# Optimization experiments

Hardware: AMD Instinct MI355X
Metric: run time of the kernel (lower is better)

The kernel has to match this reference:

```python
import jax, jax.numpy as jnp
import numpy as np

N, NPER, B, E = 65536, 1024, 64, 1048576
IN_F, HID, K, NCLS = 128, 64, 16, 10


def setup_inputs() -> dict:
    key = jax.random.key(0)
    ks = jax.random.split(key, 12)
    x = jax.random.normal(ks[0], (N, IN_F), jnp.float32)
    # block-structured intra-graph edges: 64 graphs of 1024 contiguous nodes
    gid = jax.random.randint(ks[1], (E,), 0, B)
    src = gid * NPER + jax.random.randint(ks[2], (E,), 0, NPER)
    dst = gid * NPER + jax.random.randint(ks[3], (E,), 0, NPER)
    edge_index = jnp.stack([src, dst]).astype(jnp.int32)
    batch = (jnp.arange(N, dtype=jnp.int32) // NPER).astype(jnp.int32)
    def lin(k, fo, fi):
        kw, kb = jax.random.split(k)
        s = 1.0 / np.sqrt(fi)
        return (jax.random.uniform(kw, (fo, fi), jnp.float32, -s, s),
                jax.random.uniform(kb, (fo,), jnp.float32, -s, s))
    W1, b1 = lin(ks[4], HID, IN_F)
    W2, b2 = lin(ks[5], HID, HID)
    Wp, bp = lin(ks[6], K, HID)      # DMoN cluster-assignment MLP (single Linear)
    Wl, bl = lin(ks[7], NCLS, HID)   # final classifier
    return {"x": x, "edge_index": edge_index, "batch": batch,
            "W1": W1, "b1": b1, "W2": W2, "b2": b2,
            "Wp": Wp, "bp": bp, "Wl": Wl, "bl": bl}


def gcn_conv(x, src, dst, W, b):
    # GCNConv with add_self_loops=True, symmetric normalization
    n = x.shape[0]
    deg = jax.ops.segment_sum(jnp.ones(src.shape[0], x.dtype), dst,
                              num_segments=n) + 1.0  # +1 for self-loop
    dinv = jax.lax.rsqrt(deg)
    h = x @ W.T
    coef = (dinv[src] * dinv[dst])[:, None]
    agg = jax.ops.segment_sum(h[src] * coef, dst, num_segments=n)
    agg = agg + h * (dinv * dinv)[:, None]  # self-loop contribution
    return agg + b


def reference(x, edge_index, batch, W1, b1, W2, b2, Wp, bp, Wl, bl):
    src, dst = edge_index[0], edge_index[1]
    h = jax.nn.relu(gcn_conv(x, src, dst, W1, b1))
    h = jax.nn.relu(gcn_conv(h, src, dst, W2, b2))
    # to_dense_batch: graphs are equal-sized and contiguous -> reshape, mask all True
    Xb = h.reshape(B, NPER, HID)
    # DMoN cluster assignment (dropout=0.0, mask all ones)
    s = jax.nn.softmax(Xb @ Wp.T + bp, axis=-1)          # [B, NPER, K]
    Xp = jax.nn.selu(jnp.einsum('bnk,bnh->bkh', s, Xb))   # pooled clusters [B, K, HID]
    out = Xp.mean(axis=1)                                  # [B, HID]
    logits = out @ Wl.T + bl                               # [B, NCLS]
    return logits
```

## Files before the change

### kernel.cpp

```cpp
#include <hip/hip_runtime.h>
#include <cstddef>

#define N_NODES 65536
#define NPER    1024
#define NGRAPH  64
#define HID     64
#define IN_F    128
#define KCLUS   16
#define NCLS    10
#define ECAP    18432
#define HSTRIDE 12

__global__ __launch_bounds__(256) void bucket_kernel(const int* __restrict__ src,
                                                     const int* __restrict__ dst,
                                                     int* __restrict__ ecnt,
                                                     int* __restrict__ gedges, int E) {
    __shared__ int hist[NGRAPH];
    __shared__ int base_l[NGRAPH];
    const int t = threadIdx.x;
    const int e0 = blockIdx.x * 1024;
    if (t < NGRAPH) hist[t] = 0;
    __syncthreads();

    int gg[4], rr[4], pk[4];
#pragma unroll
    for (int i = 0; i < 4; ++i) {
        int idx = e0 + i * 256 + t;
        if (idx < E) {
            int d = dst[idx], s = src[idx];
            int g = d >> 10;
            gg[i] = g;
            pk[i] = ((d & 1023) << 10) | (s & 1023);
            rr[i] = atomicAdd(&hist[g], 1);
        } else gg[i] = -1;
    }
    __syncthreads();
    if (t < NGRAPH) base_l[t] = atomicAdd(&ecnt[t], hist[t]);
    __syncthreads();
#pragma unroll
    for (int i = 0; i < 4; ++i) {
        if (gg[i] >= 0) {
            int pos = base_l[gg[i]] + rr[i];
            if (pos < ECAP) gedges[gg[i] * ECAP + pos] = pk[i];
        }
    }
}

__global__ __launch_bounds__(1024) void csr_kernel(const int* __restrict__ gedges,
                                                   const int* __restrict__ ecnt,
                                                   int* __restrict__ rp,
                                                   unsigned short* __restrict__ esorted,
                                                   float* __restrict__ dinv) {
    __shared__ int hist[NPER];
    __shared__ int wsum[16];
    const int g = blockIdx.x, t = threadIdx.x;
    const int lane = t & 63, wid = t >> 6;
    const int ec = ecnt[g];
    const int* ge = gedges + (size_t)g * ECAP;

    hist[t] = 0;
    __syncthreads();
    for (int i = t; i < ec; i += 1024) atomicAdd(&hist[ge[i] >> 10], 1);
    __syncthreads();

    const int h0 = hist[t];
    int v = h0;
#pragma unroll
    for (int off = 1; off < 64; off <<= 1) {
        int x = __shfl_up(v, off, 64);
        if (lane >= off) v += x;
    }
    if (lane == 63) wsum[wid] = v;
    __syncthreads();
    if (wid == 0) {
        int wv = (lane < 16) ? wsum[lane] : 0;
#pragma unroll
        for (int off = 1; off < 16; off <<= 1) {
            int x = __shfl_up(wv, off, 64);
            if (lane >= off) wv += x;
        }
        if (lane < 16) wsum[lane] = wv;
    }
    __syncthreads();
    const int incl = v + (wid > 0 ? wsum[wid - 1] : 0);
    const int excl = incl - h0;

    rp[g * (NPER + 1) + t] = excl;
    if (t == NPER - 1) rp[g * (NPER + 1) + NPER] = incl;
    dinv[g * NPER + t] = rsqrtf((float)h0 + 1.0f);

    hist[t] = excl;
    __syncthreads();

    unsigned short* es = esorted + (size_t)g * ECAP;
    for (int i = t; i < ec; i += 1024) {
        int pk = ge[i];
        int pos = atomicAdd(&hist[pk >> 10], 1);
        es[pos] = (unsigned short)(pk & 1023);
    }
}

template <int K>
__global__ __launch_bounds__(256) void linear_kernel(const float* __restrict__ X,
                                                     const float* __restrict__ W,
                                                     float* __restrict__ Y) {
    __shared__ float xsT[64][68];
    __shared__ float wsT[64][68];
    const int t = threadIdx.x;
    const size_t row0 = (size_t)blockIdx.x * 64;
    const int r0 = (t >> 4) * 4;
    const int c0 = (t & 15) * 4;
    float acc[4][4] = {};

    for (int kc = 0; kc < K; kc += 64) {
        __syncthreads();
        for (int i = t; i < 1024; i += 256) {
            int row = i >> 4, k4 = (i & 15) << 2;
            float4 v = *(const float4*)(X + (row0 + row) * K + kc + k4);
            xsT[k4 + 0][row] = v.x;
            xsT[k4 + 1][row] = v.y;
            xsT[k4 + 2][row] = v.z;
            xsT[k4 + 3][row] = v.w;
        }
        for (int i = t; i < 1024; i += 256) {
            int col = i >> 4, k4 = (i & 15) << 2;
            float4 v = *(const float4*)(W + col * K + kc + k4);
            wsT[k4 + 0][col] = v.x;
            wsT[k4 + 1][col] = v.y;
            wsT[k4 + 2][col] = v.z;
            wsT[k4 + 3][col] = v.w;
        }
        __syncthreads();

#pragma unroll 8
        for (int k = 0; k < 64; ++k) {
            float4 xv = *(const float4*)&xsT[k][r0];
            float4 wv = *(const float4*)&wsT[k][c0];
            acc[0][0] = fmaf(xv.x, wv.x, acc[0][0]);
            acc[0][1] = fmaf(xv.x, wv.y, acc[0][1]);
            acc[0][2] = fmaf(xv.x, wv.z, acc[0][2]);
            acc[0][3] = fmaf(xv.x, wv.w, acc[0][3]);
            acc[1][0] = fmaf(xv.y, wv.x, acc[1][0]);
            acc[1][1] = fmaf(xv.y, wv.y, acc[1][1]);
            acc[1][2] = fmaf(xv.y, wv.z, acc[1][2]);
            acc[1][3] = fmaf(xv.y, wv.w, acc[1][3]);
            acc[2][0] = fmaf(xv.z, wv.x, acc[2][0]);
            acc[2][1] = fmaf(xv.z, wv.y, acc[2][1]);
            acc[2][2] = fmaf(xv.z, wv.z, acc[2][2]);
            acc[2][3] = fmaf(xv.z, wv.w, acc[2][3]);
            acc[3][0] = fmaf(xv.w, wv.x, acc[3][0]);
            acc[3][1] = fmaf(xv.w, wv.y, acc[3][1]);
            acc[3][2] = fmaf(xv.w, wv.z, acc[3][2]);
            acc[3][3] = fmaf(xv.w, wv.w, acc[3][3]);
        }
    }

#pragma unroll
    for (int i = 0; i < 4; ++i) {
        float4 v = make_float4(acc[i][0], acc[i][1], acc[i][2], acc[i][3]);
        *(float4*)(Y + (row0 + r0 + i) * HID + c0) = v;
    }
}

__global__ __launch_bounds__(512) void agg_kernel(const float* __restrict__ h,
                                                  const unsigned short* __restrict__ esorted,
                                                  const int* __restrict__ rp,
                                                  const float* __restrict__ dinv,
                                                  const float* __restrict__ bias,
                                                  float* __restrict__ outp) {
    __shared__ float Hs[NPER * HSTRIDE];
    __shared__ float dl[NPER];
    const int g = blockIdx.x >> 3;
    const int f0 = (blockIdx.x & 7) * 8;
    const int t = threadIdx.x;
    const int base = g * NPER;

    for (int r = t; r < NPER; r += 512) {
        const float* hp = h + (size_t)(base + r) * HID + f0;
        float4 a = *(const float4*)hp;
        float4 b = *(const float4*)(hp + 4);
        float dv = dinv[base + r];
        dl[r] = dv;
        float* row = &Hs[r * HSTRIDE];
        *(float4*)row = make_float4(a.x * dv, a.y * dv, a.z * dv, a.w * dv);
        *(float4*)(row + 4) = make_float4(b.x * dv, b.y * dv, b.z * dv, b.w * dv);
    }
    float bb[8];
#pragma unroll
    for (int j = 0; j < 8; ++j) bb[j] = bias[f0 + j];
    const unsigned short* es = esorted + (size_t)g * ECAP;
    const int* rpg = rp + g * (NPER + 1);
    __syncthreads();

    for (int ld = t; ld < NPER; ld += 512) {
        int p = rpg[ld];
        const int pe = rpg[ld + 1];
        const float* srow = &Hs[ld * HSTRIDE];
        float4 acc0 = *(const float4*)srow;
        float4 acc1 = *(const float4*)(srow + 4);
        float4 bcc0 = make_float4(0.f, 0.f, 0.f, 0.f);
        float4 bcc1 = make_float4(0.f, 0.f, 0.f, 0.f);

        for (; p + 4 <= pe; p += 4) {
            const float* r0 = &Hs[(int)es[p + 0] * HSTRIDE];
            const float* r1 = &Hs[(int)es[p + 1] * HSTRIDE];
            const float* r2 = &Hs[(int)es[p + 2] * HSTRIDE];
            const float* r3 = &Hs[(int)es[p + 3] * HSTRIDE];
            float4 a0 = *(const float4*)r0, a1 = *(const float4*)(r0 + 4);
            float4 b0 = *(const float4*)r1, b1 = *(const float4*)(r1 + 4);
            float4 c0v = *(const float4*)r2, c1v = *(const float4*)(r2 + 4);
            float4 d0 = *(const float4*)r3, d1 = *(const float4*)(r3 + 4);
            acc0.x += a0.x; acc0.y += a0.y; acc0.z += a0.z; acc0.w += a0.w;
            acc1.x += a1.x; acc1.y += a1.y; acc1.z += a1.z; acc1.w += a1.w;
            bcc0.x += b0.x; bcc0.y += b0.y; bcc0.z += b0.z; bcc0.w += b0.w;
            bcc1.x += b1.x; bcc1.y += b1.y; bcc1.z += b1.z; bcc1.w += b1.w;
            acc0.x += c0v.x; acc0.y += c0v.y; acc0.z += c0v.z; acc0.w += c0v.w;
            acc1.x += c1v.x; acc1.y += c1v.y; acc1.z += c1v.z; acc1.w += c1v.w;
            bcc0.x += d0.x; bcc0.y += d0.y; bcc0.z += d0.z; bcc0.w += d0.w;
            bcc1.x += d1.x; bcc1.y += d1.y; bcc1.z += d1.z; bcc1.w += d1.w;
        }
        for (; p < pe; ++p) {
            const float* rw = &Hs[(int)es[p] * HSTRIDE];
            float4 a = *(const float4*)rw;
            float4 b = *(const float4*)(rw + 4);
            acc0.x += a.x; acc0.y += a.y; acc0.z += a.z; acc0.w += a.w;
            acc1.x += b.x; acc1.y += b.y; acc1.z += b.z; acc1.w += b.w;
        }
        acc0.x += bcc0.x; acc0.y += bcc0.y; acc0.z += bcc0.z; acc0.w += bcc0.w;
        acc1.x += bcc1.x; acc1.y += bcc1.y; acc1.z += bcc1.z; acc1.w += bcc1.w;

        const float dv = dl[ld];
        float4 o0, o1;
        o0.x = fmaxf(fmaf(acc0.x, dv, bb[0]), 0.f);
        o0.y = fmaxf(fmaf(acc0.y, dv, bb[1]), 0.f);
        o0.z = fmaxf(fmaf(acc0.z, dv, bb[2]), 0.f);
        o0.w = fmaxf(fmaf(acc0.w, dv, bb[3]), 0.f);
        o1.x = fmaxf(fmaf(acc1.x, dv, bb[4]), 0.f);
        o1.y = fmaxf(fmaf(acc1.y, dv, bb[5]), 0.f);
        o1.z = fmaxf(fmaf(acc1.z, dv, bb[6]), 0.f);
        o1.w = fmaxf(fmaf(acc1.w, dv, bb[7]), 0.f);
        float* op = outp + (size_t)(base + ld) * HID + f0;
        *(float4*)op = o0;
        *(float4*)(op + 4) = o1;
    }
}

__global__ __launch_bounds__(256) void pool1_kernel(const float* __restrict__ h,
                                                    const float* __restrict__ Wp,
                                                    const float* __restrict__ bp,
                                                    float* __restrict__ xpart) {
    __shared__ float xs[128][HID + 1];
    __shared__ float ss[128][KCLUS + 1];
    __shared__ float wp[KCLUS][HID];
    __shared__ float bps[KCLUS];
    const int g = blockIdx.x >> 3;
    const int c = blockIdx.x & 7;
    const int t = threadIdx.x;
    const float* hb = h + ((size_t)g * NPER + c * 128) * HID;

    for (int i = t; i < 128 * HID / 4; i += 256) {
        float4 v = ((const float4*)hb)[i];
        int row = i >> 4, col = (i & 15) * 4;
        xs[row][col] = v.x; xs[row][col + 1] = v.y; xs[row][col + 2] = v.z; xs[row][col + 3] = v.w;
    }
    for (int i = t; i < KCLUS * HID; i += 256) wp[i >> 6][i & 63] = Wp[i];
    if (t < KCLUS) bps[t] = bp[t];
    __syncthreads();

    if (t < 128) {
        float lg[KCLUS];
        float mx = -1e30f;
#pragma unroll
        for (int k = 0; k < KCLUS; ++k) {
            float a = bps[k];
#pragma unroll 8
            for (int hh = 0; hh < HID; ++hh) a = fmaf(xs[t][hh], wp[k][hh], a);
            lg[k] = a;
            mx = fmaxf(mx, a);
        }
        float sum = 0.f;
#pragma unroll
        for (int k = 0; k < KCLUS; ++k) {
            lg[k] = __expf(lg[k] - mx);
            sum += lg[k];
        }
        float inv = 1.0f / sum;
#pragma unroll
        for (int k = 0; k < KCLUS; ++k) ss[t][k] = lg[k] * inv;
    }
    __syncthreads();

    const int hcol = t & 63;
    const int k0 = (t >> 6) * 4;
    float a0 = 0.f, a1 = 0.f, a2 = 0.f, a3 = 0.f;
#pragma unroll 8
    for (int n = 0; n < 128; ++n) {
        float xv = xs[n][hcol];
        a0 = fmaf(ss[n][k0 + 0], xv, a0);
        a1 = fmaf(ss[n][k0 + 1], xv, a1);
        a2 = fmaf(ss[n][k0 + 2], xv, a2);
        a3 = fmaf(ss[n][k0 + 3], xv, a3);
    }
    float* xp = xpart + (((size_t)(g * 8 + c)) * KCLUS + k0) * HID + hcol;
    xp[0] = a0; xp[HID] = a1; xp[2 * HID] = a2; xp[3 * HID] = a3;
}

__global__ __launch_bounds__(256) void pool2_kernel(const float* __restrict__ xpart,
                                                    const float* __restrict__ Wl,
                                                    const float* __restrict__ bl,
                                                    float* __restrict__ out) {
    __shared__ float xp[KCLUS][HID + 1];
    __shared__ float outm[HID];
    const int g = blockIdx.x;
    const int t = threadIdx.x;
    const int hcol = t & 63;
    const int k0 = (t >> 6) * 4;
    const float* base = xpart + (size_t)g * 8 * KCLUS * HID;

    float a[4] = {};
#pragma unroll
    for (int c = 0; c < 8; ++c)
#pragma unroll
        for (int j = 0; j < 4; ++j)
            a[j] += base[(c * KCLUS + k0 + j) * HID + hcol];

    const float sc = 1.0507009873554805f, al = 1.6732632423543772f;
#pragma unroll
    for (int j = 0; j < 4; ++j) {
        float v = a[j];
        xp[k0 + j][hcol] = v > 0.f ? sc * v : sc * al * (__expf(v) - 1.f);
    }
    __syncthreads();

    if (t < HID) {
        float m = 0.f;
#pragma unroll
        for (int k = 0; k < KCLUS; ++k) m += xp[k][t];
        outm[t] = m * (1.0f / KCLUS);
    }
    __syncthreads();

    if (t < NCLS) {
        float acc = bl[t];
#pragma unroll 8
        for (int hh = 0; hh < HID; ++hh) acc = fmaf(outm[hh], Wl[t * HID + hh], acc);
        out[g * NCLS + t] = acc;
    }
}

extern "C" void kernel_launch(void* const* d_in, const int* in_sizes, int n_in,
                              void* d_out, int out_size, void* d_ws, size_t ws_size,
                              hipStream_t stream) {
    const float* x  = (const float*)d_in[0];
    const int* eidx = (const int*)d_in[1];
    const float* W1 = (const float*)d_in[3];
    const float* b1 = (const float*)d_in[4];
    const float* W2 = (const float*)d_in[5];
    const float* b2 = (const float*)d_in[6];
    const float* Wp = (const float*)d_in[7];
    const float* bp = (const float*)d_in[8];
    const float* Wl = (const float*)d_in[9];
    const float* bl = (const float*)d_in[10];
    float* out = (float*)d_out;

    const int E = in_sizes[1] / 2;
    const int* src = eidx;
    const int* dst = eidx + E;

    char* w = (char*)d_ws;
    int*            ecnt    = (int*)w;            w += 256;
    int*            gedges  = (int*)w;            w += (size_t)NGRAPH * ECAP * 4;
    unsigned short* esorted = (unsigned short*)w; w += (size_t)NGRAPH * ECAP * 2;
    int*            rp      = (int*)w;            w += (size_t)NGRAPH * (NPER + 1) * 4;
    float*          dinv    = (float*)w;          w += (size_t)N_NODES * 4;
    float*          A       = (float*)w;          w += (size_t)N_NODES * HID * 4;
    float*          Bf      = (float*)w;          w += (size_t)N_NODES * HID * 4;
    float*          xpart   = (float*)w;          w += (size_t)NGRAPH * 8 * KCLUS * HID * 4;

    hipMemsetAsync(ecnt, 0, 256, stream);
    bucket_kernel<<<(E + 1023) / 1024, 256, 0, stream>>>(src, dst, ecnt, gedges, E);
    csr_kernel<<<NGRAPH, 1024, 0, stream>>>(gedges, ecnt, rp, esorted, dinv);

    linear_kernel<IN_F><<<N_NODES / 64, 256, 0, stream>>>(x, W1, A);
    agg_kernel<<<NGRAPH * 8, 512, 0, stream>>>(A, esorted, rp, dinv, b1, Bf);

    linear_kernel<HID><<<N_NODES / 64, 256, 0, stream>>>(Bf, W2, A);
    agg_kernel<<<NGRAPH * 8, 512, 0, stream>>>(A, esorted, rp, dinv, b2, Bf);

    pool1_kernel<<<NGRAPH * 8, 256, 0, stream>>>(Bf, Wp, bp, xpart);
    pool2_kernel<<<NGRAPH, 256, 0, stream>>>(xpart, Wl, bl, out);
}
```

Baseline: 237.4 us.

## Pad CSR rows to multiples of four with zero-row sentinel, vectorize index loads

```diff
diff --git a/kernel.cpp b/kernel.cpp
--- a/kernel.cpp
+++ b/kernel.cpp
@@ -8,8 +8,9 @@
 #define IN_F    128
 #define KCLUS   16
 #define NCLS    10
-#define ECAP    18432
+#define ECAP    20480
 #define HSTRIDE 12
+#define ZROW    NPER
 
 __global__ __launch_bounds__(256) void bucket_kernel(const int* __restrict__ src,
                                                      const int* __restrict__ dst,
@@ -64,7 +65,8 @@
     __syncthreads();
 
     const int h0 = hist[t];
-    int v = h0;
+    const int pd = (h0 + 3) & ~3;
+    int v = pd;
 #pragma unroll
     for (int off = 1; off < 64; off <<= 1) {
         int x = __shfl_up(v, off, 64);
@@ -83,7 +85,7 @@
     }
     __syncthreads();
     const int incl = v + (wid > 0 ? wsum[wid - 1] : 0);
-    const int excl = incl - h0;
+    const int excl = incl - pd;
 
     rp[g * (NPER + 1) + t] = excl;
     if (t == NPER - 1) rp[g * (NPER + 1) + NPER] = incl;
@@ -98,6 +100,8 @@
         int pos = atomicAdd(&hist[pk >> 10], 1);
         es[pos] = (unsigned short)(pk & 1023);
     }
+    __syncthreads();
+    for (int q = excl + h0; q < excl + pd; ++q) es[q] = (unsigned short)ZROW;
 }
 
 template <int K>
@@ -168,10 +172,10 @@
                                                   const float* __restrict__ dinv,
                                                   const float* __restrict__ bias,
                                                   float* __restrict__ outp) {
-    __shared__ float Hs[NPER * HSTRIDE];
+    __shared__ float Hs[(NPER + 1) * HSTRIDE];
     __shared__ float dl[NPER];
-    const int g = blockIdx.x >> 3;
-    const int f0 = (blockIdx.x & 7) * 8;
+    const int g = blockIdx.x & 63;
+    const int f0 = (blockIdx.x >> 6) * 8;
     const int t = threadIdx.x;
     const int base = g * NPER;
 
@@ -185,6 +189,7 @@
         *(float4*)row = make_float4(a.x * dv, a.y * dv, a.z * dv, a.w * dv);
         *(float4*)(row + 4) = make_float4(b.x * dv, b.y * dv, b.z * dv, b.w * dv);
     }
+    if (t < HSTRIDE) Hs[ZROW * HSTRIDE + t] = 0.f;
     float bb[8];
 #pragma unroll
     for (int j = 0; j < 8; ++j) bb[j] = bias[f0 + j];
@@ -201,11 +206,12 @@
         float4 bcc0 = make_float4(0.f, 0.f, 0.f, 0.f);
         float4 bcc1 = make_float4(0.f, 0.f, 0.f, 0.f);
 
-        for (; p + 4 <= pe; p += 4) {
-            const float* r0 = &Hs[(int)es[p + 0] * HSTRIDE];
-            const float* r1 = &Hs[(int)es[p + 1] * HSTRIDE];
-            const float* r2 = &Hs[(int)es[p + 2] * HSTRIDE];
-            const float* r3 = &Hs[(int)es[p + 3] * HSTRIDE];
+        for (; p < pe; p += 4) {
+            uint2 w4 = *(const uint2*)(es + p);
+            const float* r0 = &Hs[(int)(w4.x & 0xFFFFu) * HSTRIDE];
+            const float* r1 = &Hs[(int)(w4.x >> 16) * HSTRIDE];
+            const float* r2 = &Hs[(int)(w4.y & 0xFFFFu) * HSTRIDE];
+            const float* r3 = &Hs[(int)(w4.y >> 16) * HSTRIDE];
             float4 a0 = *(const float4*)r0, a1 = *(const float4*)(r0 + 4);
             float4 b0 = *(const float4*)r1, b1 = *(const float4*)(r1 + 4);
             float4 c0v = *(const float4*)r2, c1v = *(const float4*)(r2 + 4);
@@ -218,13 +224,6 @@
             acc1.x += c1v.x; acc1.y += c1v.y; acc1.z += c1v.z; acc1.w += c1v.w;
             bcc0.x += d0.x; bcc0.y += d0.y; bcc0.z += d0.z; bcc0.w += d0.w;
             bcc1.x += d1.x; bcc1.y += d1.y; bcc1.z += d1.z; bcc1.w += d1.w;
-        }
-        for (; p < pe; ++p) {
-            const float* rw = &Hs[(int)es[p] * HSTRIDE];
-            float4 a = *(const float4*)rw;
-            float4 b = *(const float4*)(rw + 4);
-            acc0.x += a.x; acc0.y += a.y; acc0.z += a.z; acc0.w += a.w;
-            acc1.x += b.x; acc1.y += b.y; acc1.z += b.z; acc1.w += b.w;
         }
         acc0.x += bcc0.x; acc0.y += bcc0.y; acc0.z += bcc0.z; acc0.w += bcc0.w;
         acc1.x += bcc1.x; acc1.y += bcc1.y; acc1.z += bcc1.z; acc1.w += bcc1.w;
```

After: 230.6 us. -2.9%, faster.
